# Kernel tuning notes

Measured on AMD Instinct MI355X. Metric: run time of the kernel, lower is better.

Reference implementation:

```python
import jax, jax.numpy as jnp
import numpy as np

B, T, C, H, NT = 1, 1024, 768, 12, 8
D = C // H  # 64
POWER_ITERS = 4
DP_TEMP = 0.8
ESR_GAMMA = 0.02
ESR_ALPHA = 0.1


def rmsnorm(x, w, eps=1e-6):
    rms = jax.lax.rsqrt(jnp.mean(x * x, axis=-1, keepdims=True) + eps)
    return x * rms * w


def setup_inputs():
    key = jax.random.key(0)
    k0, k1, k2 = jax.random.split(key, 3)
    return {
        "x": jax.random.normal(k0, (B, T, C), jnp.float32),
        "W_qkvg": jax.random.normal(k1, (4 * C, C), jnp.float32) * 0.02,
        "W_out": jax.random.normal(k2, (C, C), jnp.float32) * 0.02,
        "lam": jnp.float32(1.5),
        "log_tau": -0.5 * jnp.ones((H, NT), jnp.float32),
        "logit_w": jnp.zeros((H, NT), jnp.float32),
        "beta": 1.5 * jnp.ones((H,), jnp.float32),
        "out_scale": jnp.ones((H,), jnp.float32),
        "dp_scale": jnp.ones((H,), jnp.float32),
        "logk_scale": jnp.ones((H,), jnp.float32),
        "dt_logit": jnp.float32(np.log(1.0 / 1e-8)),  # dt=1.0 -> logit = log(dt/(1-dt+1e-8))
        "g_norm_w": jnp.ones((D,), jnp.float32),
    }


def reference(x, W_qkvg, W_out, lam, log_tau, logit_w, beta, out_scale,
              dp_scale, logk_scale, dt_logit, g_norm_w):
    # qkvg projection and head split
    qkvg = x @ W_qkvg.T                                    # [B,T,4C]
    q, k, v, g = jnp.split(qkvg, 4, axis=-1)
    to_heads = lambda t: t.reshape(B, T, H, D).transpose(0, 2, 1, 3)  # [B,H,T,D]
    q, k, v, g = map(to_heads, (q, k, v, g))
    g = rmsnorm(g, g_norm_w)

    # pairwise squared distance ||g_i - g_j||^2
    g2 = jnp.sum(g * g, axis=-1)                           # [B,H,T]
    s = jnp.maximum(g2[..., :, None] + g2[..., None, :]
                    - 2.0 * jnp.einsum('bhid,bhjd->bhij', g, g), 0.0)  # [B,H,T,T]

    # fractional log-kernel: logsumexp_t[-(beta/2) log1p(s/(4 tau_t)) + log w_t]
    tau = jnp.maximum(jnp.exp(log_tau), 1e-6)              # [H,NT]
    w = jax.nn.softmax(logit_w, axis=-1)                   # [H,NT]
    beta_c = jnp.clip(beta, 0.5, 2.5)                      # [H]
    log_k_per = -(beta_c[None, :, None, None, None] / 2.0) * jnp.log1p(
        s[:, :, None] / (4.0 * tau[None, :, :, None, None]))          # [B,H,NT,T,T]
    logK = jax.nn.logsumexp(log_k_per + jnp.log(w + 1e-12)[None, :, :, None, None], axis=2)
    logK = logK * logk_scale[None, :, None, None]

    # dot-product scores
    dp = jnp.einsum('bhid,bhjd->bhij', q, k) * (dp_scale[None, :, None, None]
                                                / (np.sqrt(D) * DP_TEMP))

    # causal Markov normalize: blend, mask, stable row-softmax
    mask = jnp.tril(jnp.ones((T, T), bool))[None, None]    # [1,1,T,T]
    blended = lam * dp + (1.0 - lam) * logK
    blended = jnp.where(mask, blended, -jnp.inf)
    mx = jnp.max(blended, axis=-1, keepdims=True)
    mx = jnp.where(jnp.isfinite(mx), mx, 0.0)
    Kmat = jnp.exp(jnp.maximum(blended - mx, -60.0)) * mask
    P = Kmat / jnp.maximum(Kmat.sum(-1, keepdims=True), 1e-12)

    # power iteration for left stationary pi with full-support teleport
    pi0 = jnp.full((B, H, 1, T), 1.0 / T, P.dtype)
    def step(pi, _):
        p = (1.0 - ESR_GAMMA) * (pi @ P) + ESR_GAMMA / T
        p = p / jnp.maximum(p.sum(-1, keepdims=True), 1e-12)
        return p, None
    pi, _ = jax.lax.scan(step, pi0, None, length=POWER_ITERS)
    pi = jax.lax.stop_gradient(pi[..., 0, :])              # [B,H,T] (detached)

    # causal approximation to additive reversibilization
    P_adj = (pi[..., None, :] / jnp.maximum(pi[..., :, None], 1e-12)) \
            * jnp.swapaxes(P, -1, -2)                      # P*_ij = (pi_j/pi_i) P_ji
    P_rev = 0.5 * (P + P_adj) * mask
    P_rev = P_rev / jnp.maximum(P_rev.sum(-1, keepdims=True), 1e-12)

    dt = jax.nn.sigmoid(dt_logit)
    alpha = ESR_ALPHA * dt                                  # scale_alpha_by_dt=True
    P_fin = (1.0 - alpha) * P + alpha * P_rev

    y = (P_fin @ v) * out_scale[None, :, None, None]       # [B,H,T,D]
    y = y.transpose(0, 2, 1, 3).reshape(B, T, C)
    return y @ W_out.T
```

## Files before the change

### kernel.cpp

```cpp
#include <hip/hip_runtime.h>
#include <math.h>

#define TSEQ 1024
#define CD   768
#define HN   12
#define DD   64
#define CH   4

#define OFF_QH     0
#define OFF_KH     393216
#define OFF_GH     786432
#define OFF_VHT    1179648
#define OFF_VH     1572864
#define OFF_G2     1966080
#define OFF_YB     1978368
#define OFF_CONSTS 2371584
#define OFF_OPART  2372096
#define OFF_LS     5517824
#define OFF_PD     5566976
#define OFF_XB     5579264
#define OFF_WQB    5972480
#define OFF_WOB    7152128

#define NG_X  98304
#define NG_WQ 294912
#define NG_WO 73728

typedef __bf16 bf16x8 __attribute__((ext_vector_type(8)));
typedef float  f32x4  __attribute__((ext_vector_type(4)));
typedef unsigned short u16x8 __attribute__((ext_vector_type(8)));
typedef unsigned short u16x4 __attribute__((ext_vector_type(4)));

__device__ inline unsigned short f2bf(float f) {
  unsigned int u = __float_as_uint(f);
  return (unsigned short)((u + 0x7fffu + ((u >> 16) & 1u)) >> 16);
}
__device__ inline float bf2f(unsigned short u) {
  return __uint_as_float((unsigned)u << 16);
}


__global__ __launch_bounds__(256) void convert_kernel(
    const float* __restrict__ x, const float* __restrict__ wq,
    const float* __restrict__ wo, unsigned short* __restrict__ swzA,
    unsigned short* __restrict__ swzWQ, unsigned short* __restrict__ swzWO,
    const float* __restrict__ lam_p, const float* __restrict__ log_tau,
    const float* __restrict__ logit_w, const float* __restrict__ beta,
    const float* __restrict__ out_scale, const float* __restrict__ dp_scale,
    const float* __restrict__ logk_scale, const float* __restrict__ dt_logit,
    float* __restrict__ consts) {
  if (blockIdx.x == 0 && threadIdx.x < 64) {
    int h = threadIdx.x;
    if (h == 0) {
      float dt = 1.0f / (1.0f + __expf(-dt_logit[0]));
      consts[288] = 0.1f * dt;
    }
    if (h < HN) {
      float lam = lam_p[0];
      float* c = consts + h * 24;
      c[0] = lam * dp_scale[h] * (1.0f / 6.4f);
      c[1] = (1.0f - lam) * logk_scale[h];
      float b = fminf(fmaxf(beta[h], 0.5f), 2.5f);
      c[2] = 0.5f * b;
      c[3] = out_scale[h];
      float m = -1e30f;
      float lw[8];
      bool uni = true;
      for (int t = 0; t < 8; t++) {
        lw[t] = logit_w[h * 8 + t];
        m = fmaxf(m, lw[t]);
        if (log_tau[h * 8 + t] != log_tau[h * 8] || lw[t] != lw[0]) uni = false;
      }
      float s = 0.f;
      float e[8];
      for (int t = 0; t < 8; t++) { e[t] = __expf(lw[t] - m); s += e[t]; }
      for (int t = 0; t < 8; t++) {
        float w = e[t] / s;
        c[12 + t] = log2f(w + 1e-12f);
        float tau = fmaxf(__expf(log_tau[h * 8 + t]), 1e-6f);
        c[4 + t] = 1.0f / (4.0f * tau);
      }
      c[20] = uni ? 1.0f : 8.0f;
    }
  }
  int g = blockIdx.x * 256 + threadIdx.x;
  const float* src;
  unsigned short* dst;
  int lg;
  if (g < NG_X) { src = x; dst = swzA; lg = g; }
  else if (g < NG_X + NG_WQ) { src = wq; dst = swzWQ; lg = g - NG_X; }
  else if (g < NG_X + NG_WQ + NG_WO) { src = wo; dst = swzWO; lg = g - NG_X - NG_WQ; }
  else return;
  int lane = lg & 63;
  int kb = (lg >> 6) % 24;
  int t16 = lg / (64 * 24);
  int row = t16 * 16 + (lane & 15);
  int col = kb * 32 + (lane >> 4) * 8;
  const float* s = &src[(size_t)row * 768 + col];
  float4 a = *(const float4*)s;
  float4 b = *(const float4*)(s + 4);
  u16x8 u;
  u[0] = f2bf(a.x); u[1] = f2bf(a.y); u[2] = f2bf(a.z); u[3] = f2bf(a.w);
  u[4] = f2bf(b.x); u[5] = f2bf(b.y); u[6] = f2bf(b.z); u[7] = f2bf(b.w);
  *(u16x8*)&dst[(size_t)lg * 8] = u;
}

__global__ __launch_bounds__(256) void gemm_frag_qkvg(
    const unsigned short* __restrict__ swzA, const unsigned short* __restrict__ swzB,
    const float* __restrict__ consts, const float* __restrict__ g_norm_w,
    unsigned short* __restrict__ qh, unsigned short* __restrict__ kh,
    unsigned short* __restrict__ gh, unsigned short* __restrict__ vh,
    unsigned short* __restrict__ vhT, float* __restrict__ g2) {
  __shared__ __align__(16) unsigned short Ls[128 * 72];
  int t = threadIdx.x, lane = t & 63, w = t >> 6;
  int quad = lane >> 4, tx = lane & 15;
  int bid = blockIdx.x;
  int c = (bid & 7) * 48 + (bid >> 3);
  int ntile = c >> 3;
  int ybk = c & 7;
  int m0 = ybk * 128;
  int nt0 = ntile * 4;
  int mt0 = ybk * 8 + w * 2;

  f32x4 acc[2][4] = {};
#pragma unroll 2
  for (int kb = 0; kb < 24; kb++) {
    bf16x8 a0 = *(const bf16x8*)&swzA[((size_t)((mt0 + 0) * 24 + kb) * 64 + lane) * 8];
    bf16x8 a1 = *(const bf16x8*)&swzA[((size_t)((mt0 + 1) * 24 + kb) * 64 + lane) * 8];
#pragma unroll
    for (int ni = 0; ni < 4; ni++) {
      bf16x8 b = *(const bf16x8*)&swzB[((size_t)((nt0 + ni) * 24 + kb) * 64 + lane) * 8];
      acc[0][ni] = __builtin_amdgcn_mfma_f32_16x16x32_bf16(a0, b, acc[0][ni], 0, 0, 0);
      acc[1][ni] = __builtin_amdgcn_mfma_f32_16x16x32_bf16(a1, b, acc[1][ni], 0, 0, 0);
    }
  }

  int typ = ntile / 12;
  int h = ntile % 12;
  unsigned short* Lw = Ls + w * (32 * 72);
  int mrow0 = m0 + w * 32;

  if (typ == 3) {
    float gw4[4];
#pragma unroll
    for (int ni = 0; ni < 4; ni++) gw4[ni] = g_norm_w[ni * 16 + tx];
#pragma unroll
    for (int mi = 0; mi < 2; mi++) {
#pragma unroll
      for (int reg = 0; reg < 4; reg++) {
        float s1 = acc[mi][0][reg] * acc[mi][0][reg] + acc[mi][1][reg] * acc[mi][1][reg]
                 + acc[mi][2][reg] * acc[mi][2][reg] + acc[mi][3][reg] * acc[mi][3][reg];
#pragma unroll
        for (int m = 1; m < 16; m <<= 1) s1 += __shfl_xor(s1, m, 64);
        float rms = rsqrtf(s1 * (1.f / 64.f) + 1e-6f);
        int rl = mi * 16 + quad * 4 + reg;
        float s2 = 0.f;
#pragma unroll
        for (int ni = 0; ni < 4; ni++) {
          float v = acc[mi][ni][reg] * rms * gw4[ni];
          unsigned short us = f2bf(v);
          Lw[rl * 72 + ni * 16 + tx] = us;
          float vb = bf2f(us);
          s2 += vb * vb;
        }
#pragma unroll
        for (int m = 1; m < 16; m <<= 1) s2 += __shfl_xor(s2, m, 64);
        if (tx == 0) g2[h * 1024 + mrow0 + rl] = s2;
      }
    }
#pragma unroll
    for (int rep = 0; rep < 4; rep++) {
      int idx = rep * 64 + lane;
      int r = idx >> 3, cc = (idx & 7) * 8;
      *(u16x8*)&gh[(size_t)(h * 1024 + mrow0 + r) * 64 + cc] = *(const u16x8*)&Lw[r * 72 + cc];
    }
  } else {
    float sc = (typ == 0) ? consts[h * 24] * 1.44269504089f : 1.0f;
#pragma unroll
    for (int mi = 0; mi < 2; mi++)
#pragma unroll
      for (int ni = 0; ni < 4; ni++)
#pragma unroll
        for (int reg = 0; reg < 4; reg++) {
          int rl = mi * 16 + quad * 4 + reg;
          Lw[rl * 72 + ni * 16 + tx] = f2bf(acc[mi][ni][reg] * sc);
        }
    unsigned short* dst = (typ == 0) ? qh : ((typ == 1) ? kh : vh);
#pragma unroll
    for (int rep = 0; rep < 4; rep++) {
      int idx = rep * 64 + lane;
      int r = idx >> 3, cc = (idx & 7) * 8;
      *(u16x8*)&dst[(size_t)(h * 1024 + mrow0 + r) * 64 + cc] = *(const u16x8*)&Lw[r * 72 + cc];
    }
    if (typ == 2) {
#pragma unroll
      for (int rep = 0; rep < 4; rep++) {
        int idx = rep * 64 + lane;
        int d = idx >> 2, rc = (idx & 3) * 8;
        u16x8 u;
#pragma unroll
        for (int j = 0; j < 8; j++) u[j] = Lw[(rc + j) * 72 + d];
        *(u16x8*)&vhT[(size_t)(h * 64 + d) * 1024 + mrow0 + rc] = u;
      }
    }
  }
}

__global__ __launch_bounds__(256) void gemm_frag_out(
    const unsigned short* __restrict__ swzA, const unsigned short* __restrict__ swzB,
    float* __restrict__ Cm) {
  int t = threadIdx.x, lane = t & 63, w = t >> 6;
  int quad = lane >> 4, tx = lane & 15;
  int n0 = blockIdx.x * 64;
  int m0 = blockIdx.y * 128;
  int nt0 = blockIdx.x * 4;
  int mt0 = blockIdx.y * 8 + w * 2;

  f32x4 acc[2][4] = {};
#pragma unroll 2
  for (int kb = 0; kb < 24; kb++) {
    bf16x8 a0 = *(const bf16x8*)&swzA[((size_t)((mt0 + 0) * 24 + kb) * 64 + lane) * 8];
    bf16x8 a1 = *(const bf16x8*)&swzA[((size_t)((mt0 + 1) * 24 + kb) * 64 + lane) * 8];
#pragma unroll
    for (int ni = 0; ni < 4; ni++) {
      bf16x8 b = *(const bf16x8*)&swzB[((size_t)((nt0 + ni) * 24 + kb) * 64 + lane) * 8];
      acc[0][ni] = __builtin_amdgcn_mfma_f32_16x16x32_bf16(a0, b, acc[0][ni], 0, 0, 0);
      acc[1][ni] = __builtin_amdgcn_mfma_f32_16x16x32_bf16(a1, b, acc[1][ni], 0, 0, 0);
    }
  }
#pragma unroll
  for (int mi = 0; mi < 2; mi++)
#pragma unroll
    for (int ni = 0; ni < 4; ni++)
#pragma unroll
      for (int reg = 0; reg < 4; reg++) {
        int row = m0 + w * 32 + mi * 16 + quad * 4 + reg;
        Cm[(size_t)row * CD + n0 + ni * 16 + tx] = acc[mi][ni][reg];
      }
}

__global__ __launch_bounds__(256, 4) void flash_kernel(
    const unsigned short* __restrict__ qh, const unsigned short* __restrict__ kh,
    const unsigned short* __restrict__ gh, const unsigned short* __restrict__ vhT,
    const float* __restrict__ g2, const float* __restrict__ consts,
    float* __restrict__ Opart, float* __restrict__ lsp, float* __restrict__ pdp) {
  int bid = blockIdx.x;
  int cc0 = (bid & 7) * 120 + (bid >> 3);
  int h = cc0 / 80;
  int uu = 79 - (cc0 % 80);
  int it = 0, rem = uu;
  for (it = 0; it < 32; ++it) {
    int njt_ = (it >> 1) + 1;
    int nc = (njt_ + CH - 1) / CH;
    if (rem < nc) break;
    rem -= nc;
  }
  int njt = (it >> 1) + 1;
  int jt0 = rem * CH;
  int jt1 = (jt0 + CH < njt) ? (jt0 + CH) : njt;
  bool owns_diag = (jt1 == njt);
  int i0 = it * 32;
  int t = threadIdx.x;
  int lane = t & 63, w = t >> 6;
  int quad = lane >> 4, tx = lane & 15;
  int mi = w >> 1, nb = (w & 1) * 2;

  __shared__ __align__(16) unsigned short Ks[64 * 72];
  __shared__ __align__(16) unsigned short Gjs[64 * 72];
  __shared__ __align__(16) unsigned short Vt[64 * 72];
  __shared__ __align__(16) __bf16 psh[32 * 72];
  __shared__ float g2i[32], g2j[64], pdiag[32];

  const float* ch = consts + h * 24;
  float lkc = ch[1], bh2 = ch[2];
  int ntt = (int)ch[20];
  float i4t0 = ch[4];
  float cfold = -lkc * bh2;
  float m2i4 = -2.0f * i4t0;
  float g2s = (ntt == 1) ? i4t0 : 1.0f;
  float inv4tau[8], logw[8];
#pragma unroll
  for (int tt = 0; tt < 8; tt++) { inv4tau[tt] = ch[4 + tt]; logw[tt] = ch[12 + tt]; }

  int r4 = t >> 2, cb = (t & 3) * 16;

  u16x8 pk0, pk1, pg0, pg1, pv0, pv1;
  float pg2 = 0.f;
  {
    int j0 = jt0 * 64;
    const unsigned short* kp = &kh[(size_t)(h * 1024 + j0 + r4) * 64 + cb];
    const unsigned short* gp = &gh[(size_t)(h * 1024 + j0 + r4) * 64 + cb];
    const unsigned short* vp = &vhT[(size_t)(h * 64 + r4) * 1024 + j0 + cb];
    pk0 = *(const u16x8*)kp; pk1 = *(const u16x8*)(kp + 8);
    pg0 = *(const u16x8*)gp; pg1 = *(const u16x8*)(gp + 8);
    pv0 = *(const u16x8*)vp; pv1 = *(const u16x8*)(vp + 8);
    if (t < 64) pg2 = g2[h * 1024 + j0 + t];
  }

  {
    int r = t >> 3, c8 = (t & 7) * 8;
    *(u16x8*)&Ks[r * 72 + c8] = *(const u16x8*)&qh[(size_t)(h * 1024 + i0 + r) * 64 + c8];
    *(u16x8*)&Gjs[r * 72 + c8] = *(const u16x8*)&gh[(size_t)(h * 1024 + i0 + r) * 64 + c8];
  }
  if (t < 32) { g2i[t] = g2[h * 1024 + i0 + t]; pdiag[t] = 0.f; }
  __syncthreads();

  bf16x8 aq[2], ag[2];
#pragma unroll
  for (int ks = 0; ks < 2; ks++) {
    aq[ks] = *(const bf16x8*)&Ks[(mi * 16 + tx) * 72 + ks * 32 + quad * 8];
    ag[ks] = *(const bf16x8*)&Gjs[(mi * 16 + tx) * 72 + ks * 32 + quad * 8];
  }
  float g2ir[4], g2i1r[4];
#pragma unroll
  for (int reg = 0; reg < 4; reg++) {
    g2ir[reg] = g2i[mi * 16 + quad * 4 + reg];
    g2i1r[reg] = fmaf(g2ir[reg], i4t0, 1.0f);
  }

  __bf16 onebf = (__bf16)((tx == 0) ? 1.0f : 0.0f);
  bf16x8 bones = {onebf, onebf, onebf, onebf, onebf, onebf, onebf, onebf};

  f32x4 Oc[2] = {};
  f32x4 Osum = {};

  for (int jt = jt0; jt < jt1; jt++) {
    int j0 = jt * 64;
    bool masked = (jt == njt - 1);
    __syncthreads();
    *(u16x8*)&Ks[r4 * 72 + cb] = pk0;
    *(u16x8*)&Ks[r4 * 72 + cb + 8] = pk1;
    *(u16x8*)&Gjs[r4 * 72 + cb] = pg0;
    *(u16x8*)&Gjs[r4 * 72 + cb + 8] = pg1;
    *(u16x8*)&Vt[r4 * 72 + cb] = pv0;
    *(u16x8*)&Vt[r4 * 72 + cb + 8] = pv1;
    if (t < 64) g2j[t] = pg2 * g2s;
    __syncthreads();

    if (jt + 1 < jt1) {
      int jn = j0 + 64;
      const unsigned short* kp = &kh[(size_t)(h * 1024 + jn + r4) * 64 + cb];
      const unsigned short* gp = &gh[(size_t)(h * 1024 + jn + r4) * 64 + cb];
      const unsigned short* vp = &vhT[(size_t)(h * 64 + r4) * 1024 + jn + cb];
      pk0 = *(const u16x8*)kp; pk1 = *(const u16x8*)(kp + 8);
      pg0 = *(const u16x8*)gp; pg1 = *(const u16x8*)(gp + 8);
      pv0 = *(const u16x8*)vp; pv1 = *(const u16x8*)(vp + 8);
      if (t < 64) pg2 = g2[h * 1024 + jn + t];
    }

    f32x4 sqk[2] = {}, sgg[2] = {};
    __builtin_amdgcn_s_setprio(1);
#pragma unroll
    for (int ni2 = 0; ni2 < 2; ni2++) {
#pragma unroll
      for (int ks = 0; ks < 2; ks++) {
        bf16x8 bk = *(const bf16x8*)&Ks[((nb + ni2) * 16 + tx) * 72 + ks * 32 + quad * 8];
        sqk[ni2] = __builtin_amdgcn_mfma_f32_16x16x32_bf16(aq[ks], bk, sqk[ni2], 0, 0, 0);
        bf16x8 bg = *(const bf16x8*)&Gjs[((nb + ni2) * 16 + tx) * 72 + ks * 32 + quad * 8];
        sgg[ni2] = __builtin_amdgcn_mfma_f32_16x16x32_bf16(ag[ks], bg, sgg[ni2], 0, 0, 0);
      }
    }
    __builtin_amdgcn_s_setprio(0);

#pragma unroll
    for (int ni2 = 0; ni2 < 2; ni2++) {
      float g2jv = g2j[(nb + ni2) * 16 + tx];
      if (ntt == 1) {
#pragma unroll
        for (int reg = 0; reg < 4; reg++) {
          int rowl = mi * 16 + quad * 4 + reg;
          float a = fmaxf(fmaf(m2i4, sgg[ni2][reg], g2jv + g2i1r[reg]), 1.0f);
          float lv = __builtin_amdgcn_logf(a);
          float b = fmaf(cfold, lv, sqk[ni2][reg]);
          float p = __builtin_amdgcn_exp2f(b);
          if (masked) {
            int colg = j0 + (nb + ni2) * 16 + tx;
            int gi = i0 + rowl;
            if (colg > gi) p = 0.0f;
            if (colg == gi) pdiag[rowl] = p;
          }
          psh[rowl * 72 + (nb + ni2) * 16 + tx] = (__bf16)p;
        }
      } else {
#pragma unroll
        for (int reg = 0; reg < 4; reg++) {
          int rowl = mi * 16 + quad * 4 + reg;
          float s = fmaxf(g2ir[reg] + g2jv - 2.0f * sgg[ni2][reg], 0.0f);
          float se = 0.f;
#pragma unroll
          for (int tt = 0; tt < 8; tt++) {
            float lv = __builtin_amdgcn_logf(fmaf(s, inv4tau[tt], 1.0f));
            se += __builtin_amdgcn_exp2f(fmaf(-bh2, lv, logw[tt]));
          }
          float lse2 = __builtin_amdgcn_logf(se + 1e-30f);
          float b = fmaf(lkc, lse2, sqk[ni2][reg]);
          float p = __builtin_amdgcn_exp2f(b);
          if (masked) {
            int colg = j0 + (nb + ni2) * 16 + tx;
            int gi = i0 + rowl;
            if (colg > gi) p = 0.0f;
            if (colg == gi) pdiag[rowl] = p;
          }
          psh[rowl * 72 + (nb + ni2) * 16 + tx] = (__bf16)p;
        }
      }
    }
    __syncthreads();

    bf16x8 ap[2];
#pragma unroll
    for (int ks = 0; ks < 2; ks++)
      ap[ks] = *(const bf16x8*)&psh[(mi * 16 + tx) * 72 + ks * 32 + quad * 8];
    __builtin_amdgcn_s_setprio(1);
#pragma unroll
    for (int nd2 = 0; nd2 < 2; nd2++) {
#pragma unroll
      for (int ks = 0; ks < 2; ks++) {
        bf16x8 bv = *(const bf16x8*)&Vt[((nb + nd2) * 16 + tx) * 72 + ks * 32 + quad * 8];
        Oc[nd2] = __builtin_amdgcn_mfma_f32_16x16x32_bf16(ap[ks], bv, Oc[nd2], 0, 0, 0);
      }
    }
    if ((w & 1) == 0) {
#pragma unroll
      for (int ks = 0; ks < 2; ks++)
        Osum = __builtin_amdgcn_mfma_f32_16x16x32_bf16(ap[ks], bones, Osum, 0, 0, 0);
    }
    __builtin_amdgcn_s_setprio(0);
  }

  if ((w & 1) == 0 && tx == 0) {
#pragma unroll
    for (int reg = 0; reg < 4; reg++)
      lsp[(size_t)(rem * HN + h) * 1024 + i0 + mi * 16 + quad * 4 + reg] = Osum[reg];
  }
  float* Ob = Opart + (size_t)((rem * HN + h) * 1024 + i0) * 64;
#pragma unroll
  for (int nd2 = 0; nd2 < 2; nd2++) {
#pragma unroll
    for (int reg = 0; reg < 4; reg++) {
      int rowl = mi * 16 + quad * 4 + reg;
      Ob[rowl * 64 + (nb + nd2) * 16 + tx] = Oc[nd2][reg];
    }
  }
  if (owns_diag && t < 32) pdp[h * 1024 + i0 + t] = pdiag[t];
}

__global__ __launch_bounds__(256) void finalize_kernel(
    const float* __restrict__ Opart, const float* __restrict__ lsp,
    const float* __restrict__ pdp, const unsigned short* __restrict__ vh,
    const float* __restrict__ consts, unsigned short* __restrict__ yb) {
  int h = blockIdx.y;
  int t = threadIdx.x;
  int rl = t >> 4, d4 = t & 15;
  int gi = blockIdx.x * 16 + rl;
  int it = gi >> 5;
  int njt = (it >> 1) + 1;
  int nc = (njt + CH - 1) / CH;
  float alpha = consts[288];
  float osc = consts[h * 24 + 3];
  float4 Ov = make_float4(0.f, 0.f, 0.f, 0.f);
  float l = 0.f;
  for (int c = 0; c < nc; c++) {
    float4 p = *(const float4*)&Opart[(size_t)((c * HN + h) * 1024 + gi) * 64 + 4 * d4];
    Ov.x += p.x; Ov.y += p.y; Ov.z += p.z; Ov.w += p.w;
    l += lsp[(size_t)(c * HN + h) * 1024 + gi];
  }
  l = fmaxf(l, 1e-12f);
  float Pii = pdp[h * TSEQ + gi] / l;
  float inv1p = 1.0f / (1.0f + Pii);
  float c1 = (1.0f - alpha) + alpha * inv1p;
  float c2 = alpha * Pii * inv1p;
  float invl = 1.0f / l;
  u16x4 vb = *(const u16x4*)&vh[(size_t)(h * 1024 + gi) * 64 + 4 * d4];
  u16x4 o;
  o[0] = f2bf(osc * (c1 * Ov.x * invl + c2 * bf2f(vb[0])));
  o[1] = f2bf(osc * (c1 * Ov.y * invl + c2 * bf2f(vb[1])));
  o[2] = f2bf(osc * (c1 * Ov.z * invl + c2 * bf2f(vb[2])));
  o[3] = f2bf(osc * (c1 * Ov.w * invl + c2 * bf2f(vb[3])));
  int k = h * 64 + 4 * d4;
  int kb = k >> 5, q8 = (k & 31) >> 3, j0 = k & 7;
  int mt = gi >> 4, txl = gi & 15;
  size_t off = (((size_t)mt * 24 + kb) * 64 + q8 * 16 + txl) * 8 + j0;
  *(u16x4*)&yb[off] = o;
}

extern "C" void kernel_launch(void* const* d_in, const int* in_sizes, int n_in,
                              void* d_out, int out_size, void* d_ws, size_t ws_size,
                              hipStream_t stream) {
  (void)in_sizes; (void)n_in; (void)out_size; (void)ws_size;
  const float* x          = (const float*)d_in[0];
  const float* W_qkvg     = (const float*)d_in[1];
  const float* W_out      = (const float*)d_in[2];
  const float* lam        = (const float*)d_in[3];
  const float* log_tau    = (const float*)d_in[4];
  const float* logit_w    = (const float*)d_in[5];
  const float* beta       = (const float*)d_in[6];
  const float* out_scale  = (const float*)d_in[7];
  const float* dp_scale   = (const float*)d_in[8];
  const float* logk_scale = (const float*)d_in[9];
  const float* dt_logit   = (const float*)d_in[10];
  const float* g_norm_w   = (const float*)d_in[11];
  float* ws = (float*)d_ws;
  unsigned short* qh  = (unsigned short*)(ws + OFF_QH);
  unsigned short* kh  = (unsigned short*)(ws + OFF_KH);
  unsigned short* gh  = (unsigned short*)(ws + OFF_GH);
  unsigned short* vhT = (unsigned short*)(ws + OFF_VHT);
  unsigned short* vh  = (unsigned short*)(ws + OFF_VH);
  float* g2     = ws + OFF_G2;
  unsigned short* yb  = (unsigned short*)(ws + OFF_YB);
  float* consts = ws + OFF_CONSTS;
  float* Opart  = ws + OFF_OPART;
  float* lsp    = ws + OFF_LS;
  float* pdp    = ws + OFF_PD;
  unsigned short* swzA = (unsigned short*)(ws + OFF_XB);
  unsigned short* swzWQ = (unsigned short*)(ws + OFF_WQB);
  unsigned short* swzWO = (unsigned short*)(ws + OFF_WOB);
  float* out = (float*)d_out;

  convert_kernel<<<dim3((NG_X + NG_WQ + NG_WO) / 256), dim3(256), 0, stream>>>(
      x, W_qkvg, W_out, swzA, swzWQ, swzWO,
      lam, log_tau, logit_w, beta, out_scale, dp_scale, logk_scale, dt_logit, consts);
  gemm_frag_qkvg<<<dim3(384), dim3(256), 0, stream>>>(swzA, swzWQ, consts, g_norm_w,
                                                      qh, kh, gh, vh, vhT, g2);
  flash_kernel<<<dim3(960), dim3(256), 0, stream>>>(qh, kh, gh, vhT, g2, consts,
                                                    Opart, lsp, pdp);
  finalize_kernel<<<dim3(64, 12), dim3(256), 0, stream>>>(Opart, lsp, pdp, vh, consts, yb);
  gemm_frag_out<<<dim3(12, 8), dim3(256), 0, stream>>>(yb, swzWO, out);
}
```

Measured before the change: 145.1 us.

## Use 64-row query tiles per block with one warp per 16 rows

Each flash block now covers 64 query rows instead of 32, and each warp owns a full 16x64 strip. Because a warp only reads back the P rows it wrote, the barrier between writing P to shared memory and the P@V MFMA is dropped. The key-split chunk shrinks from 4 to 2 tiles, so the grid becomes 864 blocks and the Opart workspace grows. Every K/G/V tile is reused across twice as many query rows and there is one fewer barrier per tile, at the cost of more registers per warp and more partial sums for the finalize kernel to add up.

```diff
diff --git a/kernel.cpp b/kernel.cpp
--- a/kernel.cpp
+++ b/kernel.cpp
@@ -5,7 +5,7 @@
 #define CD   768
 #define HN   12
 #define DD   64
-#define CH   4
+#define CH   2
 
 #define OFF_QH     0
 #define OFF_KH     393216
@@ -16,11 +16,11 @@
 #define OFF_YB     1978368
 #define OFF_CONSTS 2371584
 #define OFF_OPART  2372096
-#define OFF_LS     5517824
-#define OFF_PD     5566976
-#define OFF_XB     5579264
-#define OFF_WQB    5972480
-#define OFF_WOB    7152128
+#define OFF_LS     8663552
+#define OFF_PD     8761856
+#define OFF_XB     8774144
+#define OFF_WQB    9167360
+#define OFF_WOB    10347008
 
 #define NG_X  98304
 #define NG_WQ 294912
@@ -245,31 +245,29 @@
     const float* __restrict__ g2, const float* __restrict__ consts,
     float* __restrict__ Opart, float* __restrict__ lsp, float* __restrict__ pdp) {
   int bid = blockIdx.x;
-  int cc0 = (bid & 7) * 120 + (bid >> 3);
-  int h = cc0 / 80;
-  int uu = 79 - (cc0 % 80);
+  int cc0 = (bid & 7) * 108 + (bid >> 3);
+  int h = cc0 / 72;
+  int uu = 71 - (cc0 % 72);
   int it = 0, rem = uu;
-  for (it = 0; it < 32; ++it) {
-    int njt_ = (it >> 1) + 1;
-    int nc = (njt_ + CH - 1) / CH;
+  for (it = 0; it < 16; ++it) {
+    int nc = (it + 2) >> 1;
     if (rem < nc) break;
     rem -= nc;
   }
-  int njt = (it >> 1) + 1;
+  int njt = it + 1;
   int jt0 = rem * CH;
   int jt1 = (jt0 + CH < njt) ? (jt0 + CH) : njt;
   bool owns_diag = (jt1 == njt);
-  int i0 = it * 32;
+  int i0 = it * 64;
   int t = threadIdx.x;
   int lane = t & 63, w = t >> 6;
   int quad = lane >> 4, tx = lane & 15;
-  int mi = w >> 1, nb = (w & 1) * 2;
 
   __shared__ __align__(16) unsigned short Ks[64 * 72];
   __shared__ __align__(16) unsigned short Gjs[64 * 72];
   __shared__ __align__(16) unsigned short Vt[64 * 72];
-  __shared__ __align__(16) __bf16 psh[32 * 72];
-  __shared__ float g2i[32], g2j[64], pdiag[32];
+  __shared__ __align__(16) __bf16 psh[64 * 72];
+  __shared__ float g2i[64], g2j[64], pdiag[64];
 
   const float* ch = consts + h * 24;
   float lkc = ch[1], bh2 = ch[2];
@@ -298,30 +296,33 @@
   }
 
   {
-    int r = t >> 3, c8 = (t & 7) * 8;
-    *(u16x8*)&Ks[r * 72 + c8] = *(const u16x8*)&qh[(size_t)(h * 1024 + i0 + r) * 64 + c8];
-    *(u16x8*)&Gjs[r * 72 + c8] = *(const u16x8*)&gh[(size_t)(h * 1024 + i0 + r) * 64 + c8];
-  }
-  if (t < 32) { g2i[t] = g2[h * 1024 + i0 + t]; pdiag[t] = 0.f; }
+    const unsigned short* qp = &qh[(size_t)(h * 1024 + i0 + r4) * 64 + cb];
+    const unsigned short* gp = &gh[(size_t)(h * 1024 + i0 + r4) * 64 + cb];
+    *(u16x8*)&Ks[r4 * 72 + cb] = *(const u16x8*)qp;
+    *(u16x8*)&Ks[r4 * 72 + cb + 8] = *(const u16x8*)(qp + 8);
+    *(u16x8*)&Gjs[r4 * 72 + cb] = *(const u16x8*)gp;
+    *(u16x8*)&Gjs[r4 * 72 + cb + 8] = *(const u16x8*)(gp + 8);
+  }
+  if (t < 64) { g2i[t] = g2[h * 1024 + i0 + t]; pdiag[t] = 0.f; }
   __syncthreads();
 
   bf16x8 aq[2], ag[2];
 #pragma unroll
   for (int ks = 0; ks < 2; ks++) {
-    aq[ks] = *(const bf16x8*)&Ks[(mi * 16 + tx) * 72 + ks * 32 + quad * 8];
-    ag[ks] = *(const bf16x8*)&Gjs[(mi * 16 + tx) * 72 + ks * 32 + quad * 8];
+    aq[ks] = *(const bf16x8*)&Ks[(w * 16 + tx) * 72 + ks * 32 + quad * 8];
+    ag[ks] = *(const bf16x8*)&Gjs[(w * 16 + tx) * 72 + ks * 32 + quad * 8];
   }
   float g2ir[4], g2i1r[4];
 #pragma unroll
   for (int reg = 0; reg < 4; reg++) {
-    g2ir[reg] = g2i[mi * 16 + quad * 4 + reg];
+    g2ir[reg] = g2i[w * 16 + quad * 4 + reg];
     g2i1r[reg] = fmaf(g2ir[reg], i4t0, 1.0f);
   }
 
   __bf16 onebf = (__bf16)((tx == 0) ? 1.0f : 0.0f);
   bf16x8 bones = {onebf, onebf, onebf, onebf, onebf, onebf, onebf, onebf};
 
-  f32x4 Oc[2] = {};
+  f32x4 Oc[4] = {};
   f32x4 Osum = {};
 
   for (int jt = jt0; jt < jt1; jt++) {
@@ -348,44 +349,44 @@
       if (t < 64) pg2 = g2[h * 1024 + jn + t];
     }
 
-    f32x4 sqk[2] = {}, sgg[2] = {};
+    f32x4 sqk[4] = {}, sgg[4] = {};
     __builtin_amdgcn_s_setprio(1);
 #pragma unroll
-    for (int ni2 = 0; ni2 < 2; ni2++) {
+    for (int nt = 0; nt < 4; nt++) {
 #pragma unroll
       for (int ks = 0; ks < 2; ks++) {
-        bf16x8 bk = *(const bf16x8*)&Ks[((nb + ni2) * 16 + tx) * 72 + ks * 32 + quad * 8];
-        sqk[ni2] = __builtin_amdgcn_mfma_f32_16x16x32_bf16(aq[ks], bk, sqk[ni2], 0, 0, 0);
-        bf16x8 bg = *(const bf16x8*)&Gjs[((nb + ni2) * 16 + tx) * 72 + ks * 32 + quad * 8];
-        sgg[ni2] = __builtin_amdgcn_mfma_f32_16x16x32_bf16(ag[ks], bg, sgg[ni2], 0, 0, 0);
+        bf16x8 bk = *(const bf16x8*)&Ks[(nt * 16 + tx) * 72 + ks * 32 + quad * 8];
+        sqk[nt] = __builtin_amdgcn_mfma_f32_16x16x32_bf16(aq[ks], bk, sqk[nt], 0, 0, 0);
+        bf16x8 bg = *(const bf16x8*)&Gjs[(nt * 16 + tx) * 72 + ks * 32 + quad * 8];
+        sgg[nt] = __builtin_amdgcn_mfma_f32_16x16x32_bf16(ag[ks], bg, sgg[nt], 0, 0, 0);
       }
     }
     __builtin_amdgcn_s_setprio(0);
 
 #pragma unroll
-    for (int ni2 = 0; ni2 < 2; ni2++) {
-      float g2jv = g2j[(nb + ni2) * 16 + tx];
+    for (int nt = 0; nt < 4; nt++) {
+      float g2jv = g2j[nt * 16 + tx];
       if (ntt == 1) {
 #pragma unroll
         for (int reg = 0; reg < 4; reg++) {
-          int rowl = mi * 16 + quad * 4 + reg;
-          float a = fmaxf(fmaf(m2i4, sgg[ni2][reg], g2jv + g2i1r[reg]), 1.0f);
+          int rowl = w * 16 + quad * 4 + reg;
+          float a = fmaxf(fmaf(m2i4, sgg[nt][reg], g2jv + g2i1r[reg]), 1.0f);
           float lv = __builtin_amdgcn_logf(a);
-          float b = fmaf(cfold, lv, sqk[ni2][reg]);
+          float b = fmaf(cfold, lv, sqk[nt][reg]);
           float p = __builtin_amdgcn_exp2f(b);
           if (masked) {
-            int colg = j0 + (nb + ni2) * 16 + tx;
+            int colg = j0 + nt * 16 + tx;
             int gi = i0 + rowl;
             if (colg > gi) p = 0.0f;
             if (colg == gi) pdiag[rowl] = p;
           }
-          psh[rowl * 72 + (nb + ni2) * 16 + tx] = (__bf16)p;
+          psh[rowl * 72 + nt * 16 + tx] = (__bf16)p;
         }
       } else {
 #pragma unroll
         for (int reg = 0; reg < 4; reg++) {
-          int rowl = mi * 16 + quad * 4 + reg;
-          float s = fmaxf(g2ir[reg] + g2jv - 2.0f * sgg[ni2][reg], 0.0f);
+          int rowl = w * 16 + quad * 4 + reg;
+          float s = fmaxf(g2ir[reg] + g2jv - 2.0f * sgg[nt][reg], 0.0f);
           float se = 0.f;
 #pragma unroll
           for (int tt = 0; tt < 8; tt++) {
@@ -393,56 +394,55 @@
             se += __builtin_amdgcn_exp2f(fmaf(-bh2, lv, logw[tt]));
           }
           float lse2 = __builtin_amdgcn_logf(se + 1e-30f);
-          float b = fmaf(lkc, lse2, sqk[ni2][reg]);
+          float b = fmaf(lkc, lse2, sqk[nt][reg]);
           float p = __builtin_amdgcn_exp2f(b);
           if (masked) {
-            int colg = j0 + (nb + ni2) * 16 + tx;
+            int colg = j0 + nt * 16 + tx;
             int gi = i0 + rowl;
             if (colg > gi) p = 0.0f;
             if (colg == gi) pdiag[rowl] = p;
           }
-          psh[rowl * 72 + (nb + ni2) * 16 + tx] = (__bf16)p;
+          psh[rowl * 72 + nt * 16 + tx] = (__bf16)p;
         }
       }
     }
+    bf16x8 ap[2];
+#pragma unroll
+    for (int ks = 0; ks < 2; ks++)
+      ap[ks] = *(const bf16x8*)&psh[(w * 16 + tx) * 72 + ks * 32 + quad * 8];
+    __builtin_amdgcn_s_setprio(1);
+#pragma unroll
+    for (int nd = 0; nd < 4; nd++) {
+#pragma unroll
+      for (int ks = 0; ks < 2; ks++) {
+        bf16x8 bv = *(const bf16x8*)&Vt[(nd * 16 + tx) * 72 + ks * 32 + quad * 8];
+        Oc[nd] = __builtin_amdgcn_mfma_f32_16x16x32_bf16(ap[ks], bv, Oc[nd], 0, 0, 0);
+      }
+    }
+#pragma unroll
+    for (int ks = 0; ks < 2; ks++)
+      Osum = __builtin_amdgcn_mfma_f32_16x16x32_bf16(ap[ks], bones, Osum, 0, 0, 0);
+    __builtin_amdgcn_s_setprio(0);
+  }
+
+  if (tx == 0) {
+#pragma unroll
+    for (int reg = 0; reg < 4; reg++)
+      lsp[(size_t)(rem * HN + h) * 1024 + i0 + w * 16 + quad * 4 + reg] = Osum[reg];
+  }
+  float* Ob = Opart + (size_t)((rem * HN + h) * 1024 + i0) * 64;
+#pragma unroll
+  for (int nd = 0; nd < 4; nd++) {
+#pragma unroll
+    for (int reg = 0; reg < 4; reg++) {
+      int rowl = w * 16 + quad * 4 + reg;
+      Ob[rowl * 64 + nd * 16 + tx] = Oc[nd][reg];
+    }
+  }
+  if (owns_diag) {
     __syncthreads();
-
-    bf16x8 ap[2];
-#pragma unroll
-    for (int ks = 0; ks < 2; ks++)
-      ap[ks] = *(const bf16x8*)&psh[(mi * 16 + tx) * 72 + ks * 32 + quad * 8];
-    __builtin_amdgcn_s_setprio(1);
-#pragma unroll
-    for (int nd2 = 0; nd2 < 2; nd2++) {
-#pragma unroll
-      for (int ks = 0; ks < 2; ks++) {
-        bf16x8 bv = *(const bf16x8*)&Vt[((nb + nd2) * 16 + tx) * 72 + ks * 32 + quad * 8];
-        Oc[nd2] = __builtin_amdgcn_mfma_f32_16x16x32_bf16(ap[ks], bv, Oc[nd2], 0, 0, 0);
-      }
-    }
-    if ((w & 1) == 0) {
-#pragma unroll
-      for (int ks = 0; ks < 2; ks++)
-        Osum = __builtin_amdgcn_mfma_f32_16x16x32_bf16(ap[ks], bones, Osum, 0, 0, 0);
-    }
-    __builtin_amdgcn_s_setprio(0);
-  }
-
-  if ((w & 1) == 0 && tx == 0) {
-#pragma unroll
-    for (int reg = 0; reg < 4; reg++)
-      lsp[(size_t)(rem * HN + h) * 1024 + i0 + mi * 16 + quad * 4 + reg] = Osum[reg];
-  }
-  float* Ob = Opart + (size_t)((rem * HN + h) * 1024 + i0) * 64;
-#pragma unroll
-  for (int nd2 = 0; nd2 < 2; nd2++) {
-#pragma unroll
-    for (int reg = 0; reg < 4; reg++) {
-      int rowl = mi * 16 + quad * 4 + reg;
-      Ob[rowl * 64 + (nb + nd2) * 16 + tx] = Oc[nd2][reg];
-    }
-  }
-  if (owns_diag && t < 32) pdp[h * 1024 + i0 + t] = pdiag[t];
+    if (t < 64) pdp[h * 1024 + i0 + t] = pdiag[t];
+  }
 }
 
 __global__ __launch_bounds__(256) void finalize_kernel(
@@ -453,8 +453,8 @@
   int t = threadIdx.x;
   int rl = t >> 4, d4 = t & 15;
   int gi = blockIdx.x * 16 + rl;
-  int it = gi >> 5;
-  int njt = (it >> 1) + 1;
+  int it = gi >> 6;
+  int njt = it + 1;
   int nc = (njt + CH - 1) / CH;
   float alpha = consts[288];
   float osc = consts[h * 24 + 3];
@@ -522,7 +522,7 @@
       lam, log_tau, logit_w, beta, out_scale, dp_scale, logk_scale, dt_logit, consts);
   gemm_frag_qkvg<<<dim3(384), dim3(256), 0, stream>>>(swzA, swzWQ, consts, g_norm_w,
                                                       qh, kh, gh, vh, vhT, g2);
-  flash_kernel<<<dim3(960), dim3(256), 0, stream>>>(qh, kh, gh, vhT, g2, consts,
+  flash_kernel<<<dim3(864), dim3(256), 0, stream>>>(qh, kh, gh, vhT, g2, consts,
                                                     Opart, lsp, pdp);
   finalize_kernel<<<dim3(64, 12), dim3(256), 0, stream>>>(Opart, lsp, pdp, vh, consts, yb);
   gemm_frag_out<<<dim3(12, 8), dim3(256), 0, stream>>>(yb, swzWO, out);
```

Measured after the change: 161.6 us. 11.4% more time.
